# Kernel optimization log

Hardware: AMD Instinct MI355X
Metric: run time of the kernel (lower is better)

The kernel has to match this reference:

```python
import jax, jax.numpy as jnp
import numpy as np

B, S, F, E, R, O = 4, 2048, 2048, 16, 16, 2048
TEMPERATURE = 1.0


def setup_inputs() -> dict:
    key = jax.random.key(0)
    k1, k2, k3, k4 = jax.random.split(key, 4)
    x = jax.random.normal(k1, (B, S, F), dtype=jnp.float32)
    prototypes = jax.random.normal(k2, (E, F), dtype=jnp.float32)
    # prototypes are top right-singular vectors -> unit norm rows
    prototypes = prototypes / jnp.linalg.norm(prototypes, axis=1, keepdims=True)
    A_stack = jax.random.normal(k3, (E, R, F), dtype=jnp.float32) * 0.02
    B_stack = jax.random.normal(k4, (E, O, R), dtype=jnp.float32) * 0.02
    scaling = jnp.float32(2.0)
    return {"x": x, "prototypes": prototypes, "A_stack": A_stack,
            "B_stack": B_stack, "scaling": scaling, "top_k": 4}


def reference(x, prototypes, A_stack, B_stack, scaling, top_k):
    lead = x.shape[:-1]
    f_in = x.shape[-1]
    tok = x.reshape(-1, f_in)                       # (t, F)
    t = tok.shape[0]

    # Arrow routing: abs cosine-like similarity to per-expert prototypes
    sim = jnp.abs(tok @ prototypes.T)               # (t, E)
    top_v, idx = jax.lax.top_k(sim, top_k)          # (t, k)
    full_score = jnp.full(sim.shape, -jnp.inf, dtype=sim.dtype)
    full_score = full_score.at[jnp.arange(t)[:, None], idx].set(top_v)
    coeff = jax.nn.softmax(full_score / TEMPERATURE, axis=1)  # (t, E), zeros off top-k

    # Per-expert LoRA: z = tok @ A_e^T  (dense over all experts, as in source)
    z = jnp.einsum('tf,erf->ter', tok, A_stack)     # (t, E, r)
    # Combine coeff into the low-rank space before the B projection to avoid
    # materializing the (t, E, out) tensor; math identical to
    # einsum('te, teo -> to', coeff, einsum('ter,eor->teo', z, B_stack)).
    delta = jnp.einsum('te,ter,eor->to', coeff, z, B_stack)  # (t, O)

    delta = scaling * delta                          # dropout = identity (eval)
    return delta.reshape(lead + (delta.shape[-1],))
```

## Files before the change

kernel.cpp:

```cpp
#include <hip/hip_runtime.h>
#include <hip/hip_bf16.h>
#include <stdint.h>

#define T_TOKENS 8192
#define F_DIM    2048
#define E_EXP    16
#define R_RANK   16
#define O_DIM    2048
#define KDIM     (E_EXP * R_RANK)

typedef short v8s __attribute__((ext_vector_type(8)));
typedef float v4f __attribute__((ext_vector_type(4)));

#define AS1 __attribute__((address_space(1)))
#define AS3 __attribute__((address_space(3)))

__device__ __forceinline__ uint16_t f2bf(float f) {
  uint32_t u = __builtin_bit_cast(uint32_t, f);
  u += 0x7fffu + ((u >> 16) & 1u);
  return (uint16_t)(u >> 16);
}

__device__ __forceinline__ void g2lds16(const void* g, void* l) {
  __builtin_amdgcn_global_load_lds((const AS1 void*)g, (AS3 void*)l, 16, 0, 0);
}

__global__ __launch_bounds__(256) void route_stream(
    const float* __restrict__ x, const float* __restrict__ P,
    const float* __restrict__ A, const float* __restrict__ Bst,
    uint16_t* __restrict__ xb, float4* __restrict__ partials4,
    uint16_t* __restrict__ Ab, uint16_t* __restrict__ Bb) {
  __shared__ float ps[16 * 256];
  const int tid = threadIdx.x;
  const int c   = blockIdx.x;
  const int by  = blockIdx.y;

  if (c == 8) {
    const int base = by * 4096;
    #pragma unroll
    for (int p = 0; p < 16; ++p) {
      const int i = base + p * 256 + tid;
      Ab[i] = f2bf(A[i]);
      const int k = i & (KDIM - 1);
      const int o = i >> 8;
      Bb[i] = f2bf(Bst[((size_t)(k >> 4) * O_DIM + o) * R_RANK + (k & 15)]);
    }
    return;
  }

  const int f0 = c * 256;
  #pragma unroll
  for (int p = 0; p < 4; ++p) {
    const int G = p * 256 + tid;
    g2lds16(&P[(size_t)(G >> 6) * F_DIM + f0 + (G & 63) * 4],
            (char*)ps + (p * 256 + (tid >> 6) * 64) * 16);
  }
  __syncthreads();

  const int sub = tid & 7;
  const int tg  = tid >> 3;
  const int r0  = by * 64 + tg;
  const int r1  = r0 + 32;
  const float* xr0 = x  + (size_t)r0 * F_DIM + f0 + sub * 4;
  const float* xr1 = x  + (size_t)r1 * F_DIM + f0 + sub * 4;
  uint16_t*    xw0 = xb + (size_t)r0 * F_DIM + f0 + sub * 4;
  uint16_t*    xw1 = xb + (size_t)r1 * F_DIM + f0 + sub * 4;
  const float* psb = ps + sub * 4;

  float a0[16], a1[16];
  #pragma unroll
  for (int e = 0; e < 16; ++e) { a0[e] = 0.f; a1[e] = 0.f; }

  float4 c0 = *(const float4*)xr0;
  float4 c1 = *(const float4*)xr1;
  #pragma unroll 1
  for (int k = 0; k < 8; ++k) {
    float4 n0, n1;
    if (k < 7) {
      n0 = *(const float4*)&xr0[(k + 1) * 32];
      n1 = *(const float4*)&xr1[(k + 1) * 32];
    }
    uint2 pk0, pk1;
    pk0.x = (uint32_t)f2bf(c0.x) | ((uint32_t)f2bf(c0.y) << 16);
    pk0.y = (uint32_t)f2bf(c0.z) | ((uint32_t)f2bf(c0.w) << 16);
    pk1.x = (uint32_t)f2bf(c1.x) | ((uint32_t)f2bf(c1.y) << 16);
    pk1.y = (uint32_t)f2bf(c1.z) | ((uint32_t)f2bf(c1.w) << 16);
    *(uint2*)&xw0[k * 32] = pk0;
    *(uint2*)&xw1[k * 32] = pk1;
    #pragma unroll
    for (int e = 0; e < 16; ++e) {
      float4 pv = *(const float4*)&psb[e * 256 + k * 32];
      a0[e] += c0.x * pv.x; a0[e] += c0.y * pv.y;
      a0[e] += c0.z * pv.z; a0[e] += c0.w * pv.w;
      a1[e] += c1.x * pv.x; a1[e] += c1.y * pv.y;
      a1[e] += c1.z * pv.z; a1[e] += c1.w * pv.w;
    }
    c0 = n0; c1 = n1;
  }

  #pragma unroll
  for (int m = 1; m <= 4; m <<= 1) {
    #pragma unroll
    for (int e = 0; e < 16; ++e) {
      a0[e] += __shfl_xor(a0[e], m, 64);
      a1[e] += __shfl_xor(a1[e], m, 64);
    }
  }

  if (sub < 4) {
    partials4[((size_t)c * 4 + sub) * T_TOKENS + r0] =
        make_float4(a0[sub * 4], a0[sub * 4 + 1], a0[sub * 4 + 2], a0[sub * 4 + 3]);
    partials4[((size_t)c * 4 + sub) * T_TOKENS + r1] =
        make_float4(a1[sub * 4], a1[sub * 4 + 1], a1[sub * 4 + 2], a1[sub * 4 + 3]);
  }
}

__global__ __launch_bounds__(256) void gemm_xa(
    const uint16_t* __restrict__ xb, const uint16_t* __restrict__ Ab,
    const float4* __restrict__ partials4, const float* __restrict__ scaling,
    const int* __restrict__ topk, uint16_t* __restrict__ wb) {
  __shared__ uint16_t S[16384];
  __shared__ float coeffL[64 * 17];
  uint16_t* Xh[2] = { S,         S + 4096  };
  uint16_t* Ah[2] = { S + 8192,  S + 12288 };
  const int tid  = threadIdx.x;
  const int b    = blockIdx.x;
  const int m_idx = (b & 7) + ((b >> 5) << 3);
  const int n_idx = (b >> 3) & 3;
  const int m0 = m_idx * 64, n0 = n_idx * 64;
  const int lane = tid & 63;
  const int wid  = tid >> 6;
  const int wm   = (wid >> 1) * 32;
  const int wn   = (wid & 1) * 32;
  const int quad = lane >> 4;
  const int cl   = lane & 15;

  if (tid < 64) {
    const int t = m0 + tid;
    double s[16];
    #pragma unroll
    for (int e = 0; e < 16; ++e) s[e] = 0.0;
    for (int c = 0; c < 8; ++c) {
      #pragma unroll
      for (int e4 = 0; e4 < 4; ++e4) {
        float4 p = partials4[((size_t)c * 4 + e4) * T_TOKENS + t];
        s[e4 * 4]     += (double)p.x;
        s[e4 * 4 + 1] += (double)p.y;
        s[e4 * 4 + 2] += (double)p.z;
        s[e4 * 4 + 3] += (double)p.w;
      }
    }
    double v[16];
    #pragma unroll
    for (int e = 0; e < 16; ++e) v[e] = fabs(s[e]);
    int k = topk[0];
    if (k > 16) k = 16;
    if (k < 1)  k = 1;
    unsigned mask = 0;
    double mx = 0.0;
    float ssum = 0.f;
    for (int i = 0; i < k; ++i) {
      double bv = -1.0; int bj = 0;
      #pragma unroll
      for (int j = 0; j < 16; ++j) {
        bool ok = !((mask >> j) & 1u) && (v[j] > bv);
        bv = ok ? v[j] : bv;
        bj = ok ? j  : bj;
      }
      mask |= 1u << bj;
      if (i == 0) mx = bv;
      ssum += expf((float)(bv - mx));
    }
    const float sc = scaling[0];
    #pragma unroll
    for (int j = 0; j < 16; ++j)
      coeffL[tid * 17 + j] = ((mask >> j) & 1u)
          ? expf((float)(v[j] - mx)) / ssum * sc : 0.f;
  }

  const int G0 = wid * 64 + lane;
  const int G1 = G0 + 256;
  const int r0 = G0 >> 3, g0 = (G0 & 7) ^ (r0 & 7);
  const int r1 = G1 >> 3, g1 = (G1 & 7) ^ (r1 & 7);
  const uint16_t* xs0 = xb + (size_t)(m0 + r0) * F_DIM + g0 * 8;
  const uint16_t* xs1 = xb + (size_t)(m0 + r1) * F_DIM + g1 * 8;
  const uint16_t* as0 = Ab + (size_t)(n0 + r0) * F_DIM + g0 * 8;
  const uint16_t* as1 = Ab + (size_t)(n0 + r1) * F_DIM + g1 * 8;
  const int d0 = wid * 512;
  const int d1 = wid * 512 + 2048;

  const int ma0 = wm + cl, ma1 = wm + 16 + cl;
  const int nb0 = wn + cl, nb1 = wn + 16 + cl;

  v4f acc[2][2];
  #pragma unroll
  for (int i = 0; i < 2; i++)
    #pragma unroll
    for (int j = 0; j < 2; j++) acc[i][j] = (v4f){0.f, 0.f, 0.f, 0.f};

  for (int k0 = 0; k0 < F_DIM; k0 += 128) {
    __syncthreads();
    g2lds16(xs0 + k0,      Xh[0] + d0);
    g2lds16(xs1 + k0,      Xh[0] + d1);
    g2lds16(as0 + k0,      Ah[0] + d0);
    g2lds16(as1 + k0,      Ah[0] + d1);
    g2lds16(xs0 + k0 + 64, Xh[1] + d0);
    g2lds16(xs1 + k0 + 64, Xh[1] + d1);
    g2lds16(as0 + k0 + 64, Ah[1] + d0);
    g2lds16(as1 + k0 + 64, Ah[1] + d1);
    __syncthreads();
    #pragma unroll
    for (int h = 0; h < 2; ++h) {
      #pragma unroll
      for (int ks = 0; ks < 2; ++ks) {
        const int gk = ks * 4 + quad;
        v8s fa0 = *(v8s*)&Xh[h][(ma0 * 8 + (gk ^ (ma0 & 7))) * 8];
        v8s fa1 = *(v8s*)&Xh[h][(ma1 * 8 + (gk ^ (ma1 & 7))) * 8];
        v8s fb0 = *(v8s*)&Ah[h][(nb0 * 8 + (gk ^ (nb0 & 7))) * 8];
        v8s fb1 = *(v8s*)&Ah[h][(nb1 * 8 + (gk ^ (nb1 & 7))) * 8];
        acc[0][0] = __builtin_amdgcn_mfma_f32_16x16x32_bf16(fa0, fb0, acc[0][0], 0, 0, 0);
        acc[0][1] = __builtin_amdgcn_mfma_f32_16x16x32_bf16(fa0, fb1, acc[0][1], 0, 0, 0);
        acc[1][0] = __builtin_amdgcn_mfma_f32_16x16x32_bf16(fa1, fb0, acc[1][0], 0, 0, 0);
        acc[1][1] = __builtin_amdgcn_mfma_f32_16x16x32_bf16(fa1, fb1, acc[1][1], 0, 0, 0);
      }
    }
  }

  __syncthreads();
  uint16_t* tile = S;
  #pragma unroll
  for (int mi = 0; mi < 2; mi++)
    #pragma unroll
    for (int ni = 0; ni < 2; ni++) {
      const int nl = wn + ni * 16 + cl;
      const int eidx = (n0 + nl) >> 4;
      #pragma unroll
      for (int reg = 0; reg < 4; reg++) {
        const int tl = wm + mi * 16 + quad * 4 + reg;
        float wv = acc[mi][ni][reg] * coeffL[tl * 17 + eidx];
        tile[tl * 72 + nl] = f2bf(wv);
      }
    }
  __syncthreads();
  #pragma unroll
  for (int p = 0; p < 2; ++p) {
    const int row  = p * 32 + (tid >> 3);
    const int colg = (tid & 7) * 8;
    uint4 val = *(uint4*)&tile[row * 72 + colg];
    *(uint4*)&wb[(size_t)(m0 + row) * KDIM + n0 + colg] = val;
  }
}

__global__ __launch_bounds__(256) void gemm_wb(
    const uint16_t* __restrict__ wbuf, const uint16_t* __restrict__ Bb,
    float* __restrict__ out) {
  __shared__ uint16_t S[20480];
  uint16_t* Ws = S;
  uint16_t* Bs = S + 4096;
  const int tid  = threadIdx.x;
  const int b    = blockIdx.x;
  const int m_idx = (b & 7) + ((b >> 6) << 3);
  const int n_idx = (b >> 3) & 7;
  const int m0 = m_idx * 64;
  const int n0 = n_idx * 256;
  const int lane = tid & 63;
  const int wid  = tid >> 6;
  const int wm   = (wid >> 1) * 32;
  const int wn   = (wid & 1) * 128;
  const int quad = lane >> 4;
  const int cl   = lane & 15;

  const int GW0 = wid * 64 + lane;
  const int GW1 = GW0 + 256;
  const int wr0 = GW0 >> 3, wg0 = (GW0 & 7) ^ (wr0 & 7);
  const int wr1 = GW1 >> 3, wg1 = (GW1 & 7) ^ (wr1 & 7);
  const uint16_t* wsrc0 = wbuf + (size_t)(m0 + wr0) * KDIM + wg0 * 8;
  const uint16_t* wsrc1 = wbuf + (size_t)(m0 + wr1) * KDIM + wg1 * 8;

  const uint16_t* bsrc[8];
  #pragma unroll
  for (int p = 0; p < 8; ++p) {
    const int G = p * 256 + wid * 64 + lane;
    const int r = G >> 3, g = (G & 7) ^ (r & 7);
    bsrc[p] = Bb + (size_t)(n0 + r) * KDIM + g * 8;
  }

  v4f acc[2][8];
  #pragma unroll
  for (int i = 0; i < 2; i++)
    #pragma unroll
    for (int j = 0; j < 8; j++) acc[i][j] = (v4f){0.f, 0.f, 0.f, 0.f};

  const int ma0 = wm + cl, ma1 = wm + 16 + cl;

  #pragma unroll
  for (int k0 = 0; k0 < KDIM; k0 += 64) {
    __syncthreads();
    g2lds16(wsrc0 + k0, Ws + wid * 512);
    g2lds16(wsrc1 + k0, Ws + wid * 512 + 2048);
    #pragma unroll
    for (int p = 0; p < 8; ++p)
      g2lds16(bsrc[p] + k0, Bs + (p * 256 + wid * 64) * 8);
    __syncthreads();
    #pragma unroll
    for (int ks = 0; ks < 2; ++ks) {
      const int gk = ks * 4 + quad;
      v8s fa0 = *(v8s*)&Ws[(ma0 * 8 + (gk ^ (ma0 & 7))) * 8];
      v8s fa1 = *(v8s*)&Ws[(ma1 * 8 + (gk ^ (ma1 & 7))) * 8];
      v8s fb[8];
      #pragma unroll
      for (int j = 0; j < 8; ++j) {
        const int nb = wn + j * 16 + cl;
        fb[j] = *(v8s*)&Bs[(nb * 8 + (gk ^ (nb & 7))) * 8];
      }
      #pragma unroll
      for (int j = 0; j < 8; ++j) {
        acc[0][j] = __builtin_amdgcn_mfma_f32_16x16x32_bf16(fa0, fb[j], acc[0][j], 0, 0, 0);
        acc[1][j] = __builtin_amdgcn_mfma_f32_16x16x32_bf16(fa1, fb[j], acc[1][j], 0, 0, 0);
      }
    }
  }

  float* ft = (float*)S;
  #pragma unroll
  for (int h = 0; h < 2; ++h) {
    __syncthreads();
    if ((wid >> 1) == h) {
      #pragma unroll
      for (int mi = 0; mi < 2; mi++)
        #pragma unroll
        for (int j = 0; j < 8; j++) {
          const int col = wn + j * 16 + cl;
          #pragma unroll
          for (int reg = 0; reg < 4; reg++) {
            const int rl = mi * 16 + quad * 4 + reg;
            ft[rl * 260 + col] = acc[mi][j][reg];
          }
        }
    }
    __syncthreads();
    #pragma unroll
    for (int p = 0; p < 8; ++p) {
      const int f4  = p * 256 + tid;
      const int row = f4 >> 6;
      const int c4  = f4 & 63;
      float4 v = *(float4*)&ft[row * 260 + c4 * 4];
      *(float4*)&out[(size_t)(m0 + h * 32 + row) * O_DIM + n0 + c4 * 4] = v;
    }
  }
}

extern "C" void kernel_launch(void* const* d_in, const int* in_sizes, int n_in,
                              void* d_out, int out_size, void* d_ws, size_t ws_size,
                              hipStream_t stream) {
  (void)in_sizes; (void)n_in; (void)out_size; (void)ws_size;
  const float* x       = (const float*)d_in[0];
  const float* P       = (const float*)d_in[1];
  const float* A       = (const float*)d_in[2];
  const float* Bst     = (const float*)d_in[3];
  const float* scaling = (const float*)d_in[4];
  const int*   topk    = (const int*)d_in[5];
  float* out = (float*)d_out;

  char* ws = (char*)d_ws;
  uint16_t* xb     = (uint16_t*)(ws);
  uint16_t* Ab     = (uint16_t*)(ws + 33554432);
  uint16_t* Bb     = (uint16_t*)(ws + 34603008);
  uint16_t* wbuf   = (uint16_t*)(ws + 35651584);
  float4*   parts  = (float4*)  (ws + 39845888);

  hipLaunchKernelGGL(route_stream, dim3(9, 128), dim3(256), 0, stream,
                     x, P, A, Bst, xb, parts, Ab, Bb);
  hipLaunchKernelGGL(gemm_xa, dim3(512), dim3(256), 0, stream,
                     xb, Ab, parts, scaling, topk, wbuf);
  hipLaunchKernelGGL(gemm_wb, dim3(1024), dim3(256), 0, stream, wbuf, Bb, out);
}
```

Baseline: 168.8 us.

## Double-buffer X/A tiles in gemm_xa and overlap routing with first load

The K loop of gemm_xa now prefetches the next 64-wide half-tile into the alternate LDS buffer while MFMAs run on the current one. Before, each iteration loaded both halves and then waited behind a barrier before computing. The top-k softmax routing per token is now spread across all four waves (16 lanes each) instead of one wave, and it runs after the first tile load is issued so that load latency is hidden. The barriers still drain all outstanding loads, so how much overlap is actually achieved depends on the compiler's waitcnt placement.

Result: no change. 171.9 us (+1.8%).

```diff
diff --git a/kernel.cpp b/kernel.cpp
--- a/kernel.cpp
+++ b/kernel.cpp
@@ -121,8 +121,10 @@
     const int* __restrict__ topk, uint16_t* __restrict__ wb) {
   __shared__ uint16_t S[16384];
   __shared__ float coeffL[64 * 17];
-  uint16_t* Xh[2] = { S,         S + 4096  };
-  uint16_t* Ah[2] = { S + 8192,  S + 12288 };
+  uint16_t* X0 = S;
+  uint16_t* X1 = S + 4096;
+  uint16_t* A0 = S + 8192;
+  uint16_t* A1 = S + 12288;
   const int tid  = threadIdx.x;
   const int b    = blockIdx.x;
   const int m_idx = (b & 7) + ((b >> 5) << 3);
@@ -135,49 +137,6 @@
   const int quad = lane >> 4;
   const int cl   = lane & 15;
 
-  if (tid < 64) {
-    const int t = m0 + tid;
-    double s[16];
-    #pragma unroll
-    for (int e = 0; e < 16; ++e) s[e] = 0.0;
-    for (int c = 0; c < 8; ++c) {
-      #pragma unroll
-      for (int e4 = 0; e4 < 4; ++e4) {
-        float4 p = partials4[((size_t)c * 4 + e4) * T_TOKENS + t];
-        s[e4 * 4]     += (double)p.x;
-        s[e4 * 4 + 1] += (double)p.y;
-        s[e4 * 4 + 2] += (double)p.z;
-        s[e4 * 4 + 3] += (double)p.w;
-      }
-    }
-    double v[16];
-    #pragma unroll
-    for (int e = 0; e < 16; ++e) v[e] = fabs(s[e]);
-    int k = topk[0];
-    if (k > 16) k = 16;
-    if (k < 1)  k = 1;
-    unsigned mask = 0;
-    double mx = 0.0;
-    float ssum = 0.f;
-    for (int i = 0; i < k; ++i) {
-      double bv = -1.0; int bj = 0;
-      #pragma unroll
-      for (int j = 0; j < 16; ++j) {
-        bool ok = !((mask >> j) & 1u) && (v[j] > bv);
-        bv = ok ? v[j] : bv;
-        bj = ok ? j  : bj;
-      }
-      mask |= 1u << bj;
-      if (i == 0) mx = bv;
-      ssum += expf((float)(bv - mx));
-    }
-    const float sc = scaling[0];
-    #pragma unroll
-    for (int j = 0; j < 16; ++j)
-      coeffL[tid * 17 + j] = ((mask >> j) & 1u)
-          ? expf((float)(v[j] - mx)) / ssum * sc : 0.f;
-  }
-
   const int G0 = wid * 64 + lane;
   const int G1 = G0 + 256;
   const int r0 = G0 >> 3, g0 = (G0 & 7) ^ (r0 & 7);
@@ -192,38 +151,87 @@
   const int ma0 = wm + cl, ma1 = wm + 16 + cl;
   const int nb0 = wn + cl, nb1 = wn + 16 + cl;
 
+#define STAGE_XA(Xb_, Ab_, kk) do {       \
+    g2lds16(xs0 + (kk), (Xb_) + d0);      \
+    g2lds16(xs1 + (kk), (Xb_) + d1);      \
+    g2lds16(as0 + (kk), (Ab_) + d0);      \
+    g2lds16(as1 + (kk), (Ab_) + d1);      \
+  } while (0)
+
+#define COMP_XA(Xb_, Ab_) do {                                                            \
+    _Pragma("unroll")                                                                     \
+    for (int ks = 0; ks < 2; ++ks) {                                                      \
+      const int gk = ks * 4 + quad;                                                       \
+      v8s fa0 = *(v8s*)&(Xb_)[(ma0 * 8 + (gk ^ (ma0 & 7))) * 8];                          \
+      v8s fa1 = *(v8s*)&(Xb_)[(ma1 * 8 + (gk ^ (ma1 & 7))) * 8];                          \
+      v8s fb0 = *(v8s*)&(Ab_)[(nb0 * 8 + (gk ^ (nb0 & 7))) * 8];                          \
+      v8s fb1 = *(v8s*)&(Ab_)[(nb1 * 8 + (gk ^ (nb1 & 7))) * 8];                          \
+      acc[0][0] = __builtin_amdgcn_mfma_f32_16x16x32_bf16(fa0, fb0, acc[0][0], 0, 0, 0);  \
+      acc[0][1] = __builtin_amdgcn_mfma_f32_16x16x32_bf16(fa0, fb1, acc[0][1], 0, 0, 0);  \
+      acc[1][0] = __builtin_amdgcn_mfma_f32_16x16x32_bf16(fa1, fb0, acc[1][0], 0, 0, 0);  \
+      acc[1][1] = __builtin_amdgcn_mfma_f32_16x16x32_bf16(fa1, fb1, acc[1][1], 0, 0, 0);  \
+    }                                                                                     \
+  } while (0)
+
   v4f acc[2][2];
   #pragma unroll
   for (int i = 0; i < 2; i++)
     #pragma unroll
     for (int j = 0; j < 2; j++) acc[i][j] = (v4f){0.f, 0.f, 0.f, 0.f};
 
+  STAGE_XA(X0, A0, 0);
+
+  if (lane < 16) {
+    const int tk = wid * 16 + cl;
+    const int t  = m0 + tk;
+    double s[16];
+    #pragma unroll
+    for (int e = 0; e < 16; ++e) s[e] = 0.0;
+    for (int c = 0; c < 8; ++c) {
+      #pragma unroll
+      for (int e4 = 0; e4 < 4; ++e4) {
+        float4 p = partials4[((size_t)c * 4 + e4) * T_TOKENS + t];
+        s[e4 * 4]     += (double)p.x;
+        s[e4 * 4 + 1] += (double)p.y;
+        s[e4 * 4 + 2] += (double)p.z;
+        s[e4 * 4 + 3] += (double)p.w;
+      }
+    }
+    double v[16];
+    #pragma unroll
+    for (int e = 0; e < 16; ++e) v[e] = fabs(s[e]);
+    int k = topk[0];
+    if (k > 16) k = 16;
+    if (k < 1)  k = 1;
+    unsigned mask = 0;
+    double mx = 0.0;
+    float ssum = 0.f;
+    for (int i = 0; i < k; ++i) {
+      double bv = -1.0; int bj = 0;
+      #pragma unroll
+      for (int j = 0; j < 16; ++j) {
+        bool ok = !((mask >> j) & 1u) && (v[j] > bv);
+        bv = ok ? v[j] : bv;
+        bj = ok ? j  : bj;
+      }
+      mask |= 1u << bj;
+      if (i == 0) mx = bv;
+      ssum += expf((float)(bv - mx));
+    }
+    const float sc = scaling[0];
+    #pragma unroll
+    for (int j = 0; j < 16; ++j)
+      coeffL[tk * 17 + j] = ((mask >> j) & 1u)
+          ? expf((float)(v[j] - mx)) / ssum * sc : 0.f;
+  }
+
   for (int k0 = 0; k0 < F_DIM; k0 += 128) {
     __syncthreads();
-    g2lds16(xs0 + k0,      Xh[0] + d0);
-    g2lds16(xs1 + k0,      Xh[0] + d1);
-    g2lds16(as0 + k0,      Ah[0] + d0);
-    g2lds16(as1 + k0,      Ah[0] + d1);
-    g2lds16(xs0 + k0 + 64, Xh[1] + d0);
-    g2lds16(xs1 + k0 + 64, Xh[1] + d1);
-    g2lds16(as0 + k0 + 64, Ah[1] + d0);
-    g2lds16(as1 + k0 + 64, Ah[1] + d1);
-    __syncthreads();
-    #pragma unroll
-    for (int h = 0; h < 2; ++h) {
-      #pragma unroll
-      for (int ks = 0; ks < 2; ++ks) {
-        const int gk = ks * 4 + quad;
-        v8s fa0 = *(v8s*)&Xh[h][(ma0 * 8 + (gk ^ (ma0 & 7))) * 8];
-        v8s fa1 = *(v8s*)&Xh[h][(ma1 * 8 + (gk ^ (ma1 & 7))) * 8];
-        v8s fb0 = *(v8s*)&Ah[h][(nb0 * 8 + (gk ^ (nb0 & 7))) * 8];
-        v8s fb1 = *(v8s*)&Ah[h][(nb1 * 8 + (gk ^ (nb1 & 7))) * 8];
-        acc[0][0] = __builtin_amdgcn_mfma_f32_16x16x32_bf16(fa0, fb0, acc[0][0], 0, 0, 0);
-        acc[0][1] = __builtin_amdgcn_mfma_f32_16x16x32_bf16(fa0, fb1, acc[0][1], 0, 0, 0);
-        acc[1][0] = __builtin_amdgcn_mfma_f32_16x16x32_bf16(fa1, fb0, acc[1][0], 0, 0, 0);
-        acc[1][1] = __builtin_amdgcn_mfma_f32_16x16x32_bf16(fa1, fb1, acc[1][1], 0, 0, 0);
-      }
-    }
+    STAGE_XA(X1, A1, k0 + 64);
+    COMP_XA(X0, A0);
+    __syncthreads();
+    if (k0 + 128 < F_DIM) STAGE_XA(X0, A0, k0 + 128);
+    COMP_XA(X1, A1);
   }
 
   __syncthreads();
@@ -249,6 +257,8 @@
     uint4 val = *(uint4*)&tile[row * 72 + colg];
     *(uint4*)&wb[(size_t)(m0 + row) * KDIM + n0 + colg] = val;
   }
+#undef STAGE_XA
+#undef COMP_XA
 }
 
 __global__ __launch_bounds__(256) void gemm_wb(
```

## Convert x to bf16 inside the XA GEMM instead of materializing a copy

Applied to the files above, without the earlier changes.

The routing kernel no longer writes a bf16 copy of x to workspace. The XA GEMM now reads fp32 x directly, converts each element to bf16 in registers and stores it into the swizzled LDS tile, while A still uses async global-to-LDS loads. This removes the bf16 write plus its later re-read, but the GEMM now reads twice as many bytes of x per tile. Those x loads are also synchronous register loads, which may expose more memory latency in the GEMM main loop. The workspace layout is compacted to match.

Result: no change. 168.9 us (+0.0%).

```diff
diff --git a/kernel.cpp b/kernel.cpp
--- a/kernel.cpp
+++ b/kernel.cpp
@@ -25,10 +25,21 @@
   __builtin_amdgcn_global_load_lds((const AS1 void*)g, (AS3 void*)l, 16, 0, 0);
 }
 
+__device__ __forceinline__ void stageX(const float* src, uint16_t* ldst) {
+  float4 a = *(const float4*)src;
+  float4 b = *(const float4*)(src + 4);
+  uint4 pk;
+  pk.x = (uint32_t)f2bf(a.x) | ((uint32_t)f2bf(a.y) << 16);
+  pk.y = (uint32_t)f2bf(a.z) | ((uint32_t)f2bf(a.w) << 16);
+  pk.z = (uint32_t)f2bf(b.x) | ((uint32_t)f2bf(b.y) << 16);
+  pk.w = (uint32_t)f2bf(b.z) | ((uint32_t)f2bf(b.w) << 16);
+  *(uint4*)ldst = pk;
+}
+
 __global__ __launch_bounds__(256) void route_stream(
     const float* __restrict__ x, const float* __restrict__ P,
     const float* __restrict__ A, const float* __restrict__ Bst,
-    uint16_t* __restrict__ xb, float4* __restrict__ partials4,
+    float4* __restrict__ partials4,
     uint16_t* __restrict__ Ab, uint16_t* __restrict__ Bb) {
   __shared__ float ps[16 * 256];
   const int tid = threadIdx.x;
@@ -61,10 +72,8 @@
   const int tg  = tid >> 3;
   const int r0  = by * 64 + tg;
   const int r1  = r0 + 32;
-  const float* xr0 = x  + (size_t)r0 * F_DIM + f0 + sub * 4;
-  const float* xr1 = x  + (size_t)r1 * F_DIM + f0 + sub * 4;
-  uint16_t*    xw0 = xb + (size_t)r0 * F_DIM + f0 + sub * 4;
-  uint16_t*    xw1 = xb + (size_t)r1 * F_DIM + f0 + sub * 4;
+  const float* xr0 = x + (size_t)r0 * F_DIM + f0 + sub * 4;
+  const float* xr1 = x + (size_t)r1 * F_DIM + f0 + sub * 4;
   const float* psb = ps + sub * 4;
 
   float a0[16], a1[16];
@@ -80,13 +89,6 @@
       n0 = *(const float4*)&xr0[(k + 1) * 32];
       n1 = *(const float4*)&xr1[(k + 1) * 32];
     }
-    uint2 pk0, pk1;
-    pk0.x = (uint32_t)f2bf(c0.x) | ((uint32_t)f2bf(c0.y) << 16);
-    pk0.y = (uint32_t)f2bf(c0.z) | ((uint32_t)f2bf(c0.w) << 16);
-    pk1.x = (uint32_t)f2bf(c1.x) | ((uint32_t)f2bf(c1.y) << 16);
-    pk1.y = (uint32_t)f2bf(c1.z) | ((uint32_t)f2bf(c1.w) << 16);
-    *(uint2*)&xw0[k * 32] = pk0;
-    *(uint2*)&xw1[k * 32] = pk1;
     #pragma unroll
     for (int e = 0; e < 16; ++e) {
       float4 pv = *(const float4*)&psb[e * 256 + k * 32];
@@ -116,7 +118,7 @@
 }
 
 __global__ __launch_bounds__(256) void gemm_xa(
-    const uint16_t* __restrict__ xb, const uint16_t* __restrict__ Ab,
+    const float* __restrict__ x, const uint16_t* __restrict__ Ab,
     const float4* __restrict__ partials4, const float* __restrict__ scaling,
     const int* __restrict__ topk, uint16_t* __restrict__ wb) {
   __shared__ uint16_t S[16384];
@@ -182,8 +184,8 @@
   const int G1 = G0 + 256;
   const int r0 = G0 >> 3, g0 = (G0 & 7) ^ (r0 & 7);
   const int r1 = G1 >> 3, g1 = (G1 & 7) ^ (r1 & 7);
-  const uint16_t* xs0 = xb + (size_t)(m0 + r0) * F_DIM + g0 * 8;
-  const uint16_t* xs1 = xb + (size_t)(m0 + r1) * F_DIM + g1 * 8;
+  const float* xs0f = x + (size_t)(m0 + r0) * F_DIM + g0 * 8;
+  const float* xs1f = x + (size_t)(m0 + r1) * F_DIM + g1 * 8;
   const uint16_t* as0 = Ab + (size_t)(n0 + r0) * F_DIM + g0 * 8;
   const uint16_t* as1 = Ab + (size_t)(n0 + r1) * F_DIM + g1 * 8;
   const int d0 = wid * 512;
@@ -200,14 +202,14 @@
 
   for (int k0 = 0; k0 < F_DIM; k0 += 128) {
     __syncthreads();
-    g2lds16(xs0 + k0,      Xh[0] + d0);
-    g2lds16(xs1 + k0,      Xh[0] + d1);
     g2lds16(as0 + k0,      Ah[0] + d0);
     g2lds16(as1 + k0,      Ah[0] + d1);
-    g2lds16(xs0 + k0 + 64, Xh[1] + d0);
-    g2lds16(xs1 + k0 + 64, Xh[1] + d1);
     g2lds16(as0 + k0 + 64, Ah[1] + d0);
     g2lds16(as1 + k0 + 64, Ah[1] + d1);
+    stageX(xs0f + k0,      Xh[0] + G0 * 8);
+    stageX(xs1f + k0,      Xh[0] + G1 * 8);
+    stageX(xs0f + k0 + 64, Xh[1] + G0 * 8);
+    stageX(xs1f + k0 + 64, Xh[1] + G1 * 8);
     __syncthreads();
     #pragma unroll
     for (int h = 0; h < 2; ++h) {
@@ -363,15 +365,14 @@
   float* out = (float*)d_out;
 
   char* ws = (char*)d_ws;
-  uint16_t* xb     = (uint16_t*)(ws);
-  uint16_t* Ab     = (uint16_t*)(ws + 33554432);
-  uint16_t* Bb     = (uint16_t*)(ws + 34603008);
-  uint16_t* wbuf   = (uint16_t*)(ws + 35651584);
-  float4*   parts  = (float4*)  (ws + 39845888);
+  uint16_t* Ab   = (uint16_t*)(ws);
+  uint16_t* Bb   = (uint16_t*)(ws + 1048576);
+  uint16_t* wbuf = (uint16_t*)(ws + 2097152);
+  float4*  parts = (float4*)  (ws + 6291456);
 
   hipLaunchKernelGGL(route_stream, dim3(9, 128), dim3(256), 0, stream,
-                     x, P, A, Bst, xb, parts, Ab, Bb);
+                     x, P, A, Bst, parts, Ab, Bb);
   hipLaunchKernelGGL(gemm_xa, dim3(512), dim3(256), 0, stream,
-                     xb, Ab, parts, scaling, topk, wbuf);
+                     x, Ab, parts, scaling, topk, wbuf);
   hipLaunchKernelGGL(gemm_wb, dim3(1024), dim3(256), 0, stream, wbuf, Bb, out);
 }
```
